# Kernel optimization log

Hardware: AMD Instinct MI355X
Metric: run time of the kernel (lower is better)

## Reference

```python
import jax, jax.numpy as jnp
import numpy as np

B, BAG, H, C = 512, 32, 1024, 53
EPS = 1e-8  # torch F.cosine_similarity denominator clamp


def setup_inputs() -> dict:
    key = jax.random.key(0)
    ks = jax.random.split(key, 5)
    return {
        "sent_reps": jax.random.normal(ks[0], (B, BAG, H), jnp.float32),
        "aug_sent_reps": jax.random.normal(ks[1], (B, BAG, H), jnp.float32),
        "rel_table": jax.random.normal(ks[2], (C, H), jnp.float32),
        "cls_w": jax.random.normal(ks[3], (C, H), jnp.float32) * 0.02,
        "cls_b": jnp.zeros((C,), jnp.float32),
        "labels": jax.random.randint(ks[4], (B,), 0, C),
        "temperature": jnp.asarray(0.1, jnp.float32),
    }


def _cl(rep, aug, bag_rep, T):
    # rep, aug: (B, bag, H); bag_rep: (B, H)
    nr = jnp.linalg.norm(rep, axis=-1)        # (B, bag)
    na = jnp.linalg.norm(aug, axis=-1)        # (B, bag)
    nb = jnp.linalg.norm(bag_rep, axis=-1)    # (B,)
    pos_sim = jnp.sum(rep * aug, axis=-1) / jnp.maximum(nr * na, EPS)  # (B, bag)
    pos = jnp.exp(pos_sim / T)
    # pair[c, j, b] = cos(rep[b, j], bag_rep[c])  -- matches torch permute/broadcast chain
    dots = jnp.einsum('bjh,ch->cjb', rep, bag_rep)               # (B, bag, B)
    denom = jnp.maximum(nb[:, None, None] * nr.T[None], EPS)      # (B, bag, B)
    pair = dots / denom
    idx = jnp.arange(rep.shape[0])
    axis_sim = pair[idx, :, idx]                                  # (B, bag): cos(rep[b,j], bag_rep[b])
    neg = jnp.exp(pair / T).sum(axis=2) - jnp.exp(axis_sim / T)   # (B, bag)
    return jnp.mean(-jnp.log(pos / (pos + neg)))


def reference(sent_reps, aug_sent_reps, rel_table, cls_w, cls_b, labels, temperature):
    # Selective attention per bag (scope slices are uniform bags of size BAG -> vectorized)
    rel = rel_table[labels]                                        # (B, H)
    scale = jnp.sqrt(jnp.asarray(H, sent_reps.dtype))
    scores = jnp.einsum('bh,bjh->bj', rel, sent_reps) / scale      # (B, bag)
    alphas = jax.nn.softmax(scores, axis=-1)
    bag_reps = jnp.einsum('bj,bjh->bh', alphas, sent_reps)         # (B, H)
    bag_out = bag_reps @ cls_w.T + cls_b                           # (B, C)  (dropout in eval = identity)
    cl_loss = _cl(sent_reps, aug_sent_reps, bag_reps, temperature)
    return bag_out, cl_loss
```

## Files before the change

kernel.cpp:

```cpp
#include <hip/hip_runtime.h>
#include <hip/hip_bf16.h>


typedef __bf16 bf16x8 __attribute__((ext_vector_type(8)));
typedef __bf16 bf16x4 __attribute__((ext_vector_type(4)));
typedef float  f32x4  __attribute__((ext_vector_type(4)));

__device__ inline float wsum(float v) {
    #pragma unroll
    for (int off = 32; off > 0; off >>= 1) v += __shfl_xor(v, off, 64);
    return v;
}

__device__ inline void gll16(const void* g, void* l) {
    __builtin_amdgcn_global_load_lds((const __attribute__((address_space(1))) void*)g,
                                     (__attribute__((address_space(3))) void*)l, 16, 0, 0);
}

__device__ inline f32x4 ntld(const float* p) {
    return __builtin_nontemporal_load((const f32x4*)p);
}

__global__ __launch_bounds__(256) void ka(
    const float* __restrict__ sent, const float* __restrict__ aug,
    const float* __restrict__ rel_table, const int* __restrict__ labels,
    __bf16* __restrict__ repb, float* __restrict__ nr, float* __restrict__ pos_sim,
    float* __restrict__ scoreg,
    const float* __restrict__ clsw, __bf16* __restrict__ cwb,
    float* __restrict__ nbsq, float* __restrict__ loss)
{
    const int t = threadIdx.x;
    if (blockIdx.x < 256) {
        const int i = blockIdx.x * 256 + t;
        cwb[i] = (i < 53 * 1024) ? (__bf16)clsw[i] : (__bf16)0.0f;
    } else if (blockIdx.x == 256) {
        nbsq[t] = 0.0f; nbsq[256 + t] = 0.0f;
        if (t == 0) *loss = 0.0f;
    }

    const int w = t >> 6, lane = t & 63;
    const int row = blockIdx.x * 4 + w;
    const int b = row >> 5;
    const size_t rbase = (size_t)row * 1024;
    const float* srow = sent + rbase;
    const float* arow = aug + rbase;
    const float* relp = rel_table + (size_t)labels[b] * 1024;

    float P = 0.f, R = 0.f, A = 0.f, D = 0.f;
    #pragma unroll
    for (int i = 0; i < 4; i++) {
        const int h = i * 256 + lane * 4;
        f32x4 v  = ntld(srow + h);
        f32x4 a  = ntld(arow + h);
        f32x4 rl = *(const f32x4*)(relp + h);
        P += v.x * rl.x + v.y * rl.y + v.z * rl.z + v.w * rl.w;
        R += v.x * v.x + v.y * v.y + v.z * v.z + v.w * v.w;
        A += a.x * a.x + a.y * a.y + a.z * a.z + a.w * a.w;
        D += v.x * a.x + v.y * a.y + v.z * a.z + v.w * a.w;
        bf16x4 vb = { (__bf16)v.x, (__bf16)v.y, (__bf16)v.z, (__bf16)v.w };
        *(bf16x4*)(repb + rbase + h) = vb;
    }
    #pragma unroll
    for (int off = 32; off > 0; off >>= 1) {
        P += __shfl_xor(P, off, 64);
        R += __shfl_xor(R, off, 64);
        A += __shfl_xor(A, off, 64);
        D += __shfl_xor(D, off, 64);
    }
    if (lane == 0) {
        scoreg[row] = P * (1.0f / 32.0f);
        float nrv = sqrtf(R), nav = sqrtf(A);
        nr[row] = nrv;
        pos_sim[row] = D / fmaxf(nrv * nav, 1e-8f);
    }
}

__global__ __launch_bounds__(256) void kb(
    const __bf16* __restrict__ repb, const float* __restrict__ scoreg,
    __bf16* __restrict__ bagb, float* __restrict__ nbsq)
{
    __shared__ float alphaS[32];
    const int b = blockIdx.x, t = threadIdx.x;
    if (t < 32) {
        float sj = scoreg[b * 32 + t];
        float m = sj;
        #pragma unroll
        for (int off = 16; off > 0; off >>= 1) m = fmaxf(m, __shfl_xor(m, off, 32));
        float e = __expf(sj - m);
        float sum = e;
        #pragma unroll
        for (int off = 16; off > 0; off >>= 1) sum += __shfl_xor(sum, off, 32);
        alphaS[t] = e / sum;
    }
    __syncthreads();

    f32x4 acc = {};
    const __bf16* base = repb + (size_t)b * 32 * 1024 + t * 4;
    #pragma unroll 8
    for (int jj = 0; jj < 32; jj++) {
        bf16x4 v = *(const bf16x4*)(base + jj * 1024);
        const float al = alphaS[jj];
        acc.x += al * (float)v.x;
        acc.y += al * (float)v.y;
        acc.z += al * (float)v.z;
        acc.w += al * (float)v.w;
    }
    bf16x4 bb = { (__bf16)acc.x, (__bf16)acc.y, (__bf16)acc.z, (__bf16)acc.w };
    *(bf16x4*)(bagb + (size_t)b * 1024 + t * 4) = bb;

    float q = acc.x * acc.x + acc.y * acc.y + acc.z * acc.z + acc.w * acc.w;
    q = wsum(q);
    if ((t & 63) == 0) atomicAdd(&nbsq[b], q);
}

__global__ __launch_bounds__(256) void k4_gemm(
    const __bf16* __restrict__ repb, const __bf16* __restrict__ bagb,
    const float* __restrict__ nr, const float* __restrict__ nbsq,
    const float* __restrict__ temp, float* __restrict__ partial, float* __restrict__ diag,
    const __bf16* __restrict__ cwb, const float* __restrict__ bias, float* __restrict__ out)
{
    __shared__ __align__(16) char smem[49152];
    __bf16* Al = (__bf16*)smem;
    __bf16* Bl = (__bf16*)(smem + 8192);
    const int bid = blockIdx.x;
    const int t = threadIdx.x, lane = t & 63, w = t >> 6;
    const int m = lane & 15, quad = lane >> 4;

    if (bid >= 512) {
        const int r0 = (bid - 512) * 64;
        f32x4 acc[4] = {};
        const int i0 = t * 8;
        const int row0 = i0 >> 5, kk0 = i0 & 31;
        const __bf16* gA = bagb + (size_t)(r0 + row0) * 1024 + kk0;
        const __bf16* gB = cwb + (size_t)row0 * 1024 + kk0;
        for (int k0 = 0; k0 < 1024; k0 += 64) {
            __syncthreads();
            gll16(gA + k0,      Al + i0);
            gll16(gA + k0 + 32, Al + 2048 + i0);
            gll16(gB + k0,      Bl + i0);
            gll16(gB + k0 + 32, Bl + 2048 + i0);
            __syncthreads();
            #pragma unroll
            for (int ks = 0; ks < 2; ks++) {
                bf16x8 a = *(const bf16x8*)(&Al[ks * 2048 + (w * 16 + m) * 32 + quad * 8]);
                #pragma unroll
                for (int n = 0; n < 4; n++) {
                    bf16x8 bf = *(const bf16x8*)(&Bl[ks * 2048 + (n * 16 + m) * 32 + quad * 8]);
                    acc[n] = __builtin_amdgcn_mfma_f32_16x16x32_bf16(a, bf, acc[n], 0, 0, 0);
                }
            }
        }
        #pragma unroll
        for (int n = 0; n < 4; n++) {
            const int c = n * 16 + m;
            if (c < 53) {
                #pragma unroll
                for (int i = 0; i < 4; i++) {
                    const int r = r0 + w * 16 + quad * 4 + i;
                    out[(size_t)r * 53 + c] = acc[n][i] + bias[c];
                }
            }
        }
        return;
    }

    float (*negp)[32][128] = (float (*)[32][128])(smem + 16384);
    const int xcd = bid & 7, slot = bid >> 3;
    const int cb = slot & 3, rb = (slot >> 2) * 8 + xcd;
    const int r0 = rb * 128, c0 = cb * 128;
    const int wr0 = (w & 1) * 64, wc0 = (w >> 1) * 64;
    const int half = w & 1;

    #pragma unroll
    for (int z = 0; z < 32; z++) ((float*)negp)[z * 256 + t] = 0.f;

    f32x4 acc[4][4] = {};

    const int i0 = t * 8, i1 = 2048 + t * 8;
    const int row0 = i0 >> 5, kk0 = i0 & 31;
    const int row1 = i1 >> 5, kk1 = i1 & 31;
    const __bf16* gA0 = repb + (size_t)(r0 + row0) * 1024 + kk0;
    const __bf16* gA1 = repb + (size_t)(r0 + row1) * 1024 + kk1;
    const __bf16* gB0 = bagb + (size_t)(c0 + row0) * 1024 + kk0;
    const __bf16* gB1 = bagb + (size_t)(c0 + row1) * 1024 + kk1;

    for (int k0 = 0; k0 < 1024; k0 += 32) {
        __syncthreads();
        gll16(gA0 + k0, Al + i0);
        gll16(gA1 + k0, Al + i1);
        gll16(gB0 + k0, Bl + i0);
        gll16(gB1 + k0, Bl + i1);
        __syncthreads();
        bf16x8 a[4], bf[4];
        #pragma unroll
        for (int i = 0; i < 4; i++) a[i]  = *(const bf16x8*)(&Al[(wr0 + i * 16 + m) * 32 + quad * 8]);
        #pragma unroll
        for (int n = 0; n < 4; n++) bf[n] = *(const bf16x8*)(&Bl[(wc0 + n * 16 + m) * 32 + quad * 8]);
        #pragma unroll
        for (int i = 0; i < 4; i++)
            #pragma unroll
            for (int n = 0; n < 4; n++)
                acc[i][n] = __builtin_amdgcn_mfma_f32_16x16x32_bf16(a[i], bf[n], acc[i][n], 0, 0, 0);
    }

    const float invT = 1.0f / *temp;
    float nrv[16];
    #pragma unroll
    for (int i = 0; i < 4; i++)
        #pragma unroll
        for (int g = 0; g < 4; g++)
            nrv[i * 4 + g] = nr[r0 + wr0 + i * 16 + quad * 4 + g];

    #pragma unroll
    for (int n = 0; n < 4; n++) {
        const int c_local = wc0 + n * 16 + m;
        const int cg = c0 + c_local;
        const float nbv = sqrtf(nbsq[cg]);
        #pragma unroll
        for (int i = 0; i < 2; i++) {
            #pragma unroll
            for (int g = 0; g < 4; g++) {
                const int jj = i * 16 + quad * 4 + g;
                const int rg0 = r0 + wr0 + i * 16 + quad * 4 + g;
                const int rg2 = rg0 + 32;
                float e0 = __expf(acc[i][n][g]     / fmaxf(nbv * nrv[i * 4 + g],       1e-8f) * invT);
                float e2 = __expf(acc[i + 2][n][g] / fmaxf(nbv * nrv[(i + 2) * 4 + g], 1e-8f) * invT);
                negp[half][jj][c_local] = e0 + e2;
                if ((rg0 >> 5) == cg) diag[(size_t)cg * 32 + jj] = e0;
                if ((rg2 >> 5) == cg) diag[(size_t)cg * 32 + jj] = e2;
            }
        }
    }
    __syncthreads();

    float* pout = partial + (size_t)rb * 32 * 512 + c0;
    #pragma unroll
    for (int v = 0; v < 4; v++) {
        const int idx = v * 1024 + t * 4;
        const int jj = idx >> 7, cl = idx & 127;
        f32x4 a = *(const f32x4*)(&negp[0][jj][cl]);
        f32x4 bq = *(const f32x4*)(&negp[1][jj][cl]);
        f32x4 s = a + bq;
        *(f32x4*)(pout + (size_t)jj * 512 + cl) = s;
    }
}

__global__ __launch_bounds__(256) void k5_neg(
    const float* __restrict__ partial, const float* __restrict__ diag,
    const float* __restrict__ pos_sim, const float* __restrict__ temp,
    float* __restrict__ loss)
{
    const int ct = blockIdx.x & 7, j = blockIdx.x >> 3;
    const int t = threadIdx.x, lane = t & 63, w = t >> 6;
    const int bsub = t >> 4;
    const int cidx = t & 15;
    f32x4 acc = {};
    #pragma unroll 4
    for (int r = 0; r < 8; r++) {
        const int rb = bsub * 8 + r;
        f32x4 v = *(const f32x4*)(partial + ((size_t)rb * 32 + j) * 512 + ct * 64 + cidx * 4);
        acc += v;
    }
    #pragma unroll
    for (int k = 0; k < 4; k++) {
        acc[k] += __shfl_xor(acc[k], 16, 64);
        acc[k] += __shfl_xor(acc[k], 32, 64);
    }
    __shared__ float red[4][64];
    if (lane < 16) {
        #pragma unroll
        for (int k = 0; k < 4; k++) red[w][lane * 4 + k] = acc[k];
    }
    __syncthreads();

    if (t < 64) {
        const int c = ct * 64 + t;
        float S = red[0][t] + red[1][t] + red[2][t] + red[3][t];
        S -= diag[(size_t)c * 32 + j];
        const float invT = 1.0f / *temp;
        const float lp = pos_sim[(c << 5) + j] * invT;
        float term = logf(__expf(lp) + S) - lp;
        term = wsum(term);
        if (t == 0) atomicAdd(loss, term * (1.0f / 16384.0f));
    }
}

extern "C" void kernel_launch(void* const* d_in, const int* in_sizes, int n_in,
                              void* d_out, int out_size, void* d_ws, size_t ws_size,
                              hipStream_t stream)
{
    const float* sent = (const float*)d_in[0];
    const float* aug  = (const float*)d_in[1];
    const float* rel  = (const float*)d_in[2];
    const float* clsw = (const float*)d_in[3];
    const float* clsb = (const float*)d_in[4];
    const int*   lab  = (const int*)d_in[5];
    const float* temp = (const float*)d_in[6];
    float* out = (float*)d_out;

    char* ws = (char*)d_ws;
    __bf16* bagb    = (__bf16*)(ws);
    float*  nbsq    = (float*)(ws + (1u << 20));
    float*  nr      = (float*)(ws + (1u << 20) + 64 * 1024);
    float*  pos     = (float*)(ws + (1u << 20) + 128 * 1024);
    __bf16* cwb     = (__bf16*)(ws + (1u << 20) + 192 * 1024);
    float*  scoreg  = (float*)(ws + (1u << 20) + 320 * 1024);
    float*  diag    = (float*)(ws + (2u << 20) + 64 * 1024);
    __bf16* repb    = (__bf16*)(ws + (4u << 20));
    float*  partial = (float*)(ws + (36u << 20));

    float* loss = out + 27136;

    ka     <<<4096, 256, 0, stream>>>(sent, aug, rel, lab, repb, nr, pos, scoreg,
                                      clsw, cwb, nbsq, loss);
    kb     <<<512, 256, 0, stream>>>(repb, scoreg, bagb, nbsq);
    k4_gemm<<<520, 256, 0, stream>>>(repb, bagb, nr, nbsq, temp, partial, diag,
                                     cwb, clsb, out);
    k5_neg <<<256, 256, 0, stream>>>(partial, diag, pos, temp, loss);
}
```

Baseline: 202.9 us.

## Double-buffer k4 GEMM LDS with 64-wide K stages and drop LDS neg reduction

Restructures the main k4 GEMM loop to use two LDS buffers with 64-deep K tiles and an MFMA-fragment-friendly layout. The next stage's global-to-LDS load is issued while the current one is being computed, which halves the number of barriers. The epilogue no longer sums the two wave halves in LDS; each half writes its own partial row block straight to global memory. The k5 reduction then sums twice as many partials, trading more global traffic and larger LDS use (64KB) for fewer syncs and less shared-memory work.

New measurement: 212.8 us. 4.9% more time.

```diff
diff --git a/kernel.cpp b/kernel.cpp
--- a/kernel.cpp
+++ b/kernel.cpp
@@ -119,14 +119,14 @@
     const float* __restrict__ temp, float* __restrict__ partial, float* __restrict__ diag,
     const __bf16* __restrict__ cwb, const float* __restrict__ bias, float* __restrict__ out)
 {
-    __shared__ __align__(16) char smem[49152];
-    __bf16* Al = (__bf16*)smem;
-    __bf16* Bl = (__bf16*)(smem + 8192);
+    __shared__ __align__(16) char smem[65536];
     const int bid = blockIdx.x;
     const int t = threadIdx.x, lane = t & 63, w = t >> 6;
     const int m = lane & 15, quad = lane >> 4;
 
     if (bid >= 512) {
+        __bf16* Al = (__bf16*)smem;
+        __bf16* Bl = (__bf16*)(smem + 8192);
         const int r0 = (bid - 512) * 64;
         f32x4 acc[4] = {};
         const int i0 = t * 8;
@@ -164,43 +164,63 @@
         return;
     }
 
-    float (*negp)[32][128] = (float (*)[32][128])(smem + 16384);
+    __bf16* A0 = (__bf16*)smem;
+    __bf16* B0 = (__bf16*)(smem + 16384);
+    __bf16* A1 = (__bf16*)(smem + 32768);
+    __bf16* B1 = (__bf16*)(smem + 49152);
+
     const int xcd = bid & 7, slot = bid >> 3;
     const int cb = slot & 3, rb = (slot >> 2) * 8 + xcd;
     const int r0 = rb * 128, c0 = cb * 128;
     const int wr0 = (w & 1) * 64, wc0 = (w >> 1) * 64;
-    const int half = w & 1;
-
-    #pragma unroll
-    for (int z = 0; z < 32; z++) ((float*)negp)[z * 256 + t] = 0.f;
+
+    int rowo[4], colo[4], ldso[4];
+    #pragma unroll
+    for (int u = 0; u < 4; u++) {
+        const int s = u * 256 + t;
+        rowo[u] = (s >> 7) * 16 + (s & 15);
+        colo[u] = ((s >> 6) & 1) * 32 + ((s >> 4) & 3) * 8;
+        ldso[u] = s * 8;
+    }
+    const __bf16* gA = repb + (size_t)r0 * 1024;
+    const __bf16* gB = bagb + (size_t)c0 * 1024;
 
     f32x4 acc[4][4] = {};
 
-    const int i0 = t * 8, i1 = 2048 + t * 8;
-    const int row0 = i0 >> 5, kk0 = i0 & 31;
-    const int row1 = i1 >> 5, kk1 = i1 & 31;
-    const __bf16* gA0 = repb + (size_t)(r0 + row0) * 1024 + kk0;
-    const __bf16* gA1 = repb + (size_t)(r0 + row1) * 1024 + kk1;
-    const __bf16* gB0 = bagb + (size_t)(c0 + row0) * 1024 + kk0;
-    const __bf16* gB1 = bagb + (size_t)(c0 + row1) * 1024 + kk1;
-
-    for (int k0 = 0; k0 < 1024; k0 += 32) {
+    auto STAGE = [&](__bf16* Ad, __bf16* Bd, int k0) {
+        #pragma unroll
+        for (int u = 0; u < 4; u++) {
+            gll16(gA + (size_t)rowo[u] * 1024 + k0 + colo[u], Ad + ldso[u]);
+            gll16(gB + (size_t)rowo[u] * 1024 + k0 + colo[u], Bd + ldso[u]);
+        }
+    };
+    auto COMPUTE = [&](const __bf16* Ar, const __bf16* Br) {
+        #pragma unroll
+        for (int ks = 0; ks < 2; ks++) {
+            bf16x8 a[4], bq[4];
+            #pragma unroll
+            for (int i = 0; i < 4; i++)
+                a[i] = *(const bf16x8*)(Ar + (((wr0 >> 4) + i) * 128 + ks * 64 + quad * 16 + m) * 8);
+            #pragma unroll
+            for (int n = 0; n < 4; n++)
+                bq[n] = *(const bf16x8*)(Br + (((wc0 >> 4) + n) * 128 + ks * 64 + quad * 16 + m) * 8);
+            #pragma unroll
+            for (int i = 0; i < 4; i++)
+                #pragma unroll
+                for (int n = 0; n < 4; n++)
+                    acc[i][n] = __builtin_amdgcn_mfma_f32_16x16x32_bf16(a[i], bq[n], acc[i][n], 0, 0, 0);
+        }
+    };
+
+    STAGE(A0, B0, 0);
+    __syncthreads();
+    for (int k0 = 0; k0 < 1024; k0 += 128) {
+        STAGE(A1, B1, k0 + 64);
+        COMPUTE(A0, B0);
         __syncthreads();
-        gll16(gA0 + k0, Al + i0);
-        gll16(gA1 + k0, Al + i1);
-        gll16(gB0 + k0, Bl + i0);
-        gll16(gB1 + k0, Bl + i1);
+        if (k0 + 128 < 1024) STAGE(A0, B0, k0 + 128);
+        COMPUTE(A1, B1);
         __syncthreads();
-        bf16x8 a[4], bf[4];
-        #pragma unroll
-        for (int i = 0; i < 4; i++) a[i]  = *(const bf16x8*)(&Al[(wr0 + i * 16 + m) * 32 + quad * 8]);
-        #pragma unroll
-        for (int n = 0; n < 4; n++) bf[n] = *(const bf16x8*)(&Bl[(wc0 + n * 16 + m) * 32 + quad * 8]);
-        #pragma unroll
-        for (int i = 0; i < 4; i++)
-            #pragma unroll
-            for (int n = 0; n < 4; n++)
-                acc[i][n] = __builtin_amdgcn_mfma_f32_16x16x32_bf16(a[i], bf[n], acc[i][n], 0, 0, 0);
     }
 
     const float invT = 1.0f / *temp;
@@ -210,6 +230,9 @@
         #pragma unroll
         for (int g = 0; g < 4; g++)
             nrv[i * 4 + g] = nr[r0 + wr0 + i * 16 + quad * 4 + g];
+
+    const int rb2 = rb * 2 + (w & 1);
+    float* pbase = partial + (size_t)rb2 * 32 * 512;
 
     #pragma unroll
     for (int n = 0; n < 4; n++) {
@@ -225,23 +248,11 @@
                 const int rg2 = rg0 + 32;
                 float e0 = __expf(acc[i][n][g]     / fmaxf(nbv * nrv[i * 4 + g],       1e-8f) * invT);
                 float e2 = __expf(acc[i + 2][n][g] / fmaxf(nbv * nrv[(i + 2) * 4 + g], 1e-8f) * invT);
-                negp[half][jj][c_local] = e0 + e2;
+                pbase[(size_t)jj * 512 + cg] = e0 + e2;
                 if ((rg0 >> 5) == cg) diag[(size_t)cg * 32 + jj] = e0;
                 if ((rg2 >> 5) == cg) diag[(size_t)cg * 32 + jj] = e2;
             }
         }
-    }
-    __syncthreads();
-
-    float* pout = partial + (size_t)rb * 32 * 512 + c0;
-    #pragma unroll
-    for (int v = 0; v < 4; v++) {
-        const int idx = v * 1024 + t * 4;
-        const int jj = idx >> 7, cl = idx & 127;
-        f32x4 a = *(const f32x4*)(&negp[0][jj][cl]);
-        f32x4 bq = *(const f32x4*)(&negp[1][jj][cl]);
-        f32x4 s = a + bq;
-        *(f32x4*)(pout + (size_t)jj * 512 + cl) = s;
     }
 }
 
@@ -256,8 +267,8 @@
     const int cidx = t & 15;
     f32x4 acc = {};
     #pragma unroll 4
-    for (int r = 0; r < 8; r++) {
-        const int rb = bsub * 8 + r;
+    for (int r = 0; r < 16; r++) {
+        const int rb = bsub * 16 + r;
         f32x4 v = *(const f32x4*)(partial + ((size_t)rb * 32 + j) * 512 + ct * 64 + cidx * 4);
         acc += v;
     }
```

## Triple-buffer the cosine GEMM K-loop with swizzled LDS and vmcnt fences

Applied to the files above, without the earlier changes.

The main pairwise-similarity GEMM blocks now use a three-stage LDS ring with async global-to-LDS loads issued two steps ahead. Each step waits with an explicit vmcnt and a single barrier, replacing the old load-then-wait-then-compute loop that had two syncs per step. Tiles are laid out with an XOR swizzle to cut LDS bank conflicts on the MFMA operand reads, and the redundant zeroing of the negative-sum scratch is dropped. LDS use grows to 64KB per block, and the scratch now aliases one of the staging buffers, which could lower occupancy.

After: 199.4 us. Within noise of the previous version (-1.7%).

```diff
diff --git a/kernel.cpp b/kernel.cpp
--- a/kernel.cpp
+++ b/kernel.cpp
@@ -119,14 +119,14 @@
     const float* __restrict__ temp, float* __restrict__ partial, float* __restrict__ diag,
     const __bf16* __restrict__ cwb, const float* __restrict__ bias, float* __restrict__ out)
 {
-    __shared__ __align__(16) char smem[49152];
-    __bf16* Al = (__bf16*)smem;
-    __bf16* Bl = (__bf16*)(smem + 8192);
+    __shared__ __align__(16) char smem[65536];
     const int bid = blockIdx.x;
     const int t = threadIdx.x, lane = t & 63, w = t >> 6;
     const int m = lane & 15, quad = lane >> 4;
 
     if (bid >= 512) {
+        __bf16* Al = (__bf16*)smem;
+        __bf16* Bl = (__bf16*)(smem + 8192);
         const int r0 = (bid - 512) * 64;
         f32x4 acc[4] = {};
         const int i0 = t * 8;
@@ -164,44 +164,62 @@
         return;
     }
 
-    float (*negp)[32][128] = (float (*)[32][128])(smem + 16384);
+    __bf16* Bu0 = (__bf16*)smem;
+    __bf16* Bu1 = (__bf16*)(smem + 16384);
+    __bf16* Bu2 = (__bf16*)(smem + 32768);
+    float (*negp)[32][128] = (float (*)[32][128])(smem + 32768);
+
     const int xcd = bid & 7, slot = bid >> 3;
     const int cb = slot & 3, rb = (slot >> 2) * 8 + xcd;
     const int r0 = rb * 128, c0 = cb * 128;
     const int wr0 = (w & 1) * 64, wc0 = (w >> 1) * 64;
     const int half = w & 1;
 
-    #pragma unroll
-    for (int z = 0; z < 32; z++) ((float*)negp)[z * 256 + t] = 0.f;
+    const int swc = 8 * ((t & 3) ^ ((t >> 3) & 3));
+    const size_t sOff = (size_t)(t >> 2) * 1024 + swc;
+    const __bf16* pA0 = repb + (size_t)r0 * 1024 + sOff;
+    const __bf16* pA1 = pA0 + 64 * 1024;
+    const __bf16* pB0 = bagb + (size_t)c0 * 1024 + sOff;
+    const __bf16* pB1 = pB0 + 64 * 1024;
+    const int d0 = t * 8, d1 = 2048 + t * 8, d2 = 4096 + t * 8, d3 = 6144 + t * 8;
+
+    const int rho = (m >> 1) & 3;
+    const int offA = ((wr0 + m) * 4 + (quad ^ rho)) * 8;
+    const int offB = 4096 + ((wc0 + m) * 4 + (quad ^ rho)) * 8;
 
     f32x4 acc[4][4] = {};
 
-    const int i0 = t * 8, i1 = 2048 + t * 8;
-    const int row0 = i0 >> 5, kk0 = i0 & 31;
-    const int row1 = i1 >> 5, kk1 = i1 & 31;
-    const __bf16* gA0 = repb + (size_t)(r0 + row0) * 1024 + kk0;
-    const __bf16* gA1 = repb + (size_t)(r0 + row1) * 1024 + kk1;
-    const __bf16* gB0 = bagb + (size_t)(c0 + row0) * 1024 + kk0;
-    const __bf16* gB1 = bagb + (size_t)(c0 + row1) * 1024 + kk1;
-
-    for (int k0 = 0; k0 < 1024; k0 += 32) {
-        __syncthreads();
-        gll16(gA0 + k0, Al + i0);
-        gll16(gA1 + k0, Al + i1);
-        gll16(gB0 + k0, Bl + i0);
-        gll16(gB1 + k0, Bl + i1);
-        __syncthreads();
-        bf16x8 a[4], bf[4];
-        #pragma unroll
-        for (int i = 0; i < 4; i++) a[i]  = *(const bf16x8*)(&Al[(wr0 + i * 16 + m) * 32 + quad * 8]);
-        #pragma unroll
-        for (int n = 0; n < 4; n++) bf[n] = *(const bf16x8*)(&Bl[(wc0 + n * 16 + m) * 32 + quad * 8]);
-        #pragma unroll
-        for (int i = 0; i < 4; i++)
-            #pragma unroll
-            for (int n = 0; n < 4; n++)
-                acc[i][n] = __builtin_amdgcn_mfma_f32_16x16x32_bf16(a[i], bf[n], acc[i][n], 0, 0, 0);
-    }
+    #define STG(buf, s) do { const int kk_ = (s) * 32;                      \
+        gll16(pA0 + kk_, (buf) + d0); gll16(pA1 + kk_, (buf) + d1);         \
+        gll16(pB0 + kk_, (buf) + d2); gll16(pB1 + kk_, (buf) + d3); } while (0)
+
+    #define CMP(buf) do { bf16x8 av_[4], bv_[4];                            \
+        _Pragma("unroll") for (int i_ = 0; i_ < 4; i_++)                    \
+            av_[i_] = *(const bf16x8*)((buf) + offA + i_ * 512);            \
+        _Pragma("unroll") for (int n_ = 0; n_ < 4; n_++)                    \
+            bv_[n_] = *(const bf16x8*)((buf) + offB + n_ * 512);            \
+        _Pragma("unroll") for (int i_ = 0; i_ < 4; i_++)                    \
+        _Pragma("unroll") for (int n_ = 0; n_ < 4; n_++)                    \
+            acc[i_][n_] = __builtin_amdgcn_mfma_f32_16x16x32_bf16(          \
+                av_[i_], bv_[n_], acc[i_][n_], 0, 0, 0); } while (0)
+
+    #define FENCE(N) do { __builtin_amdgcn_sched_barrier(0);                \
+        asm volatile("s_waitcnt vmcnt(" #N ")" ::: "memory");               \
+        __builtin_amdgcn_s_barrier();                                       \
+        __builtin_amdgcn_sched_barrier(0); } while (0)
+
+    STG(Bu0, 0);
+    STG(Bu1, 1);
+    FENCE(4);
+    #pragma unroll 1
+    for (int s = 0; s < 28; s += 3) {
+        STG(Bu2, s + 2); CMP(Bu0); FENCE(4);
+        STG(Bu0, s + 3); CMP(Bu1); FENCE(4);
+        STG(Bu1, s + 4); CMP(Bu2); FENCE(4);
+    }
+    CMP(Bu0);
+    FENCE(0);
+    CMP(Bu1);
 
     const float invT = 1.0f / *temp;
     float nrv[16];
@@ -243,6 +261,9 @@
         f32x4 s = a + bq;
         *(f32x4*)(pout + (size_t)jj * 512 + cl) = s;
     }
+    #undef STG
+    #undef CMP
+    #undef FENCE
 }
 
 __global__ __launch_bounds__(256) void k5_neg(
```
